# Kernel optimization log

Measured on AMD Instinct MI355X. Metric: run time of the kernel, lower is better.

Reference implementation:

```python
import jax, jax.numpy as jnp
import numpy as np

H1 = 768
H2 = 768
B, LQ, LK = 8, 1024, 1024


def setup_inputs() -> dict:
    key = jax.random.key(0)
    ks = jax.random.split(key, 12)
    s1 = 1.0 / np.sqrt(H1)
    s2 = 1.0 / np.sqrt(H2)
    # weights stored as [in, out] (equivalent to torch Linear weight.T)
    return {
        "tensor1": jax.random.normal(ks[0], (B, LQ, H1), jnp.float32),
        "tensor2": jax.random.normal(ks[1], (B, LK, H2), jnp.float32),
        "Wq": jax.random.uniform(ks[2], (3, H1, H2), jnp.float32, -s1, s1),
        "bq": jax.random.uniform(ks[3], (3, H2), jnp.float32, -s1, s1),
        "Wk": jax.random.uniform(ks[4], (3, H2, H2), jnp.float32, -s2, s2),
        "bk": jax.random.uniform(ks[5], (3, H2), jnp.float32, -s2, s2),
        "Wv": jax.random.uniform(ks[6], (3, H2, H2), jnp.float32, -s2, s2),
        "bv": jax.random.uniform(ks[7], (3, H2), jnp.float32, -s2, s2),
        "Wp": jax.random.uniform(ks[8], (3 * H2, H2), jnp.float32, -1.0 / np.sqrt(3 * H2), 1.0 / np.sqrt(3 * H2)),
        "bp": jax.random.uniform(ks[9], (H2,), jnp.float32, -1.0 / np.sqrt(3 * H2), 1.0 / np.sqrt(3 * H2)),
    }


def reference(tensor1, tensor2, Wq, bq, Wk, bk, Wv, bv, Wp, bp):
    # Three independent cross-attention heads, stacked on leading axis h=3.
    q = jnp.einsum("bqd,hde->hbqe", tensor1, Wq) + bq[:, None, None, :]  # [3,B,LQ,H2]
    k = jnp.einsum("bkd,hde->hbke", tensor2, Wk) + bk[:, None, None, :]  # [3,B,LK,H2]
    v = jnp.einsum("bkd,hde->hbke", tensor2, Wv) + bv[:, None, None, :]  # [3,B,LK,H2]
    scores = jnp.einsum("hbqe,hbke->hbqk", q, k)  # NOTE: no 1/sqrt(d) scaling, per original
    weights = jax.nn.softmax(scores, axis=-1)
    ctx = jnp.einsum("hbqk,hbke->hbqe", weights, v)  # [3,B,LQ,H2]
    # concat heads along feature dim -> [B,LQ,3*H2]
    multi = jnp.transpose(ctx, (1, 2, 0, 3)).reshape(ctx.shape[1], ctx.shape[2], -1)
    # project_multihead: ReLU then Linear
    return jax.nn.relu(multi) @ Wp + bp
```

## Files before the change

kernel.cpp:

```cpp
#include <hip/hip_runtime.h>
#include <hip/hip_bf16.h>


typedef _Float16 f16;
typedef __attribute__((ext_vector_type(8))) _Float16 f16x8;
typedef __attribute__((ext_vector_type(4))) float f32x4;
typedef __attribute__((ext_vector_type(4))) short s16x4;

#define DI __device__ __forceinline__

DI short f2hs(float f){
  f16 h = (f16)f;
  return __builtin_bit_cast(short, h);
}
DI float hs2f(short s){
  return (float)__builtin_bit_cast(f16, s);
}

DI f32x4 mfma16(f16x8 a, f16x8 b, f32x4 c){
  return __builtin_amdgcn_mfma_f32_16x16x32_f16(a, b, c, 0, 0, 0);
}

#define GLL16(gp, lp) __builtin_amdgcn_global_load_lds( \
    (const __attribute__((address_space(1))) unsigned int*)(gp), \
    (__attribute__((address_space(3))) unsigned int*)(lp), 16, 0, 0)

__global__ void pre_fused_kernel(
    const float* __restrict__ t1, const float* __restrict__ t2,
    short* __restrict__ t1b, short* __restrict__ t2b,
    const float* __restrict__ Wq, const float* __restrict__ Wk,
    short* __restrict__ WqH, short* __restrict__ WkH,
    const float* __restrict__ Wv, const float* __restrict__ Wp,
    short* __restrict__ WvT, short* __restrict__ WpT,
    const float* __restrict__ bq, float* __restrict__ wvb)
{
  __shared__ float tile[32][33];
  int bid = blockIdx.x;
  const int tid = threadIdx.x;

  if (bid < 12288){
    int i = bid*256 + tid;
    const float* in = (i < 1572864) ? t1 : t2;
    short* out = (i < 1572864) ? t1b : t2b;
    int j = (i < 1572864) ? i : i - 1572864;
    f32x4 v = ((const f32x4*)in)[j];
    s16x4 o;
    o[0]=f2hs(v[0]); o[1]=f2hs(v[1]); o[2]=f2hs(v[2]); o[3]=f2hs(v[3]);
    ((s16x4*)out)[j] = o;
    return;
  }
  bid -= 12288;
  if (bid < 3456){
    int i = bid*256 + tid;
    const float* in = (i < 442368) ? Wq : Wk;
    short* out = (i < 442368) ? WqH : WkH;
    int j = (i < 442368) ? i : i - 442368;
    f32x4 v = ((const f32x4*)in)[j];
    s16x4 o;
    o[0]=f2hs(v[0]); o[1]=f2hs(v[1]); o[2]=f2hs(v[2]); o[3]=f2hs(v[3]);
    ((s16x4*)out)[j] = o;
    return;
  }
  bid -= 3456;
  if (bid < 3456){
    const int bz = bid / 1728, rem = bid % 1728;
    const int by = rem / 24, bx = rem % 24;
    const float* in; short* out; int R, r0;
    if (bz == 0){
      int hd = by / 24;
      in = Wv + (long)hd*768*768; out = WvT + (long)hd*768*768;
      R = 768; r0 = (by % 24) * 32;
    } else {
      in = Wp; out = WpT; R = 2304; r0 = by * 32;
    }
    int c0 = bx * 32;
    int tx = tid & 31, ty = tid >> 5;
    #pragma unroll
    for (int k=0;k<4;k++)
      tile[ty + k*8][tx] = in[(long)(r0 + ty + k*8) * 768 + c0 + tx];
    __syncthreads();
    #pragma unroll
    for (int k=0;k<4;k++)
      out[(long)(c0 + ty + k*8) * R + r0 + tx] = f2hs(tile[tx][ty + k*8]);
    return;
  }
  bid -= 3456;
  {
    const int h = bid / 8, chunk = bid % 8;
    const int wave = tid>>6, lane = tid&63;
    const float* bql = bq + h*768 + lane*12;
    float bv[12];
    #pragma unroll
    for (int e=0;e<12;e++) bv[e] = bql[e];
    for (int r = 0; r < 24; r++){
      int d = chunk*96 + r*4 + wave;
      const float* row = Wk + ((long)h*768 + d)*768 + lane*12;
      float s = 0.f;
      #pragma unroll
      for (int e=0;e<12;e++) s += row[e] * bv[e];
      s += __shfl_xor(s, 1);
      s += __shfl_xor(s, 2);
      s += __shfl_xor(s, 4);
      s += __shfl_xor(s, 8);
      s += __shfl_xor(s, 16);
      s += __shfl_xor(s, 32);
      if (lane == 0) wvb[h*768 + d] = s;
    }
  }
}

DI void gemm_tile64(const short* __restrict__ A, const short* __restrict__ Bt, int K,
                    int m0, int n0, short* As, short* Bs, f32x4 (&acc)[4][4])
{
  const int tid = threadIdx.x, wave = tid>>6, lane = tid&63;
  const int wm = wave>>1, wn = wave&1;
  const int fl = lane&15, fq = lane>>4;
  const int srow = lane>>2;
  const int scol = ((lane&3) ^ ((lane>>3)&3))*8;
  const int rs   = (fq ^ ((fl>>1)&3))*8;
  for (int kk=0; kk<K; kk+=64){
    __syncthreads();
    #pragma unroll
    for (int c=0;c<2;c++)
      #pragma unroll
      for (int r=0;r<2;r++){
        const int rb = r*64 + wave*16;
        GLL16(A  + (long)(m0+rb+srow)*K + kk + c*32 + scol, As + c*4096 + rb*32);
        GLL16(Bt + (long)(n0+rb+srow)*K + kk + c*32 + scol, Bs + c*4096 + rb*32);
      }
    __syncthreads();
    #pragma unroll
    for (int c=0;c<2;c++){
      f16x8 a[4];
      #pragma unroll
      for (int i=0;i<4;i++) a[i] = *(const f16x8*)(As + c*4096 + (wm*64+i*16+fl)*32 + rs);
      #pragma unroll
      for (int j=0;j<4;j++){
        f16x8 b = *(const f16x8*)(Bs + c*4096 + (wn*64+j*16+fl)*32 + rs);
        #pragma unroll
        for (int i=0;i<4;i++) acc[i][j] = mfma16(a[i], b, acc[i][j]);
      }
    }
  }
}

__global__ __launch_bounds__(256,2) void gemm_m_kernel(
    const short* __restrict__ WqH, const short* __restrict__ WkH, short* __restrict__ Mt)
{
  __shared__ short As[8192];
  __shared__ short Bs[8192];
  const int h = blockIdx.z;
  const int m0 = blockIdx.x*128, n0 = blockIdx.y*128;
  const int tid = threadIdx.x, wave = tid>>6, lane = tid&63;
  const int wm = wave>>1, wn = wave&1;
  const int fl = lane&15, fq = lane>>4;

  f32x4 vz = {0.f,0.f,0.f,0.f};
  f32x4 acc[4][4];
  #pragma unroll
  for (int i=0;i<4;i++)
    #pragma unroll
    for (int j=0;j<4;j++) acc[i][j] = vz;

  gemm_tile64(WqH + (long)h*768*768, WkH + (long)h*768*768, 768, m0, n0, As, Bs, acc);

  short* outp = Mt + (long)h*768*768;
  #pragma unroll
  for (int j=0;j<4;j++){
    int col = n0 + wn*64 + j*16 + fl;
    #pragma unroll
    for (int i=0;i<4;i++){
      int row = m0 + wm*64 + i*16 + fq*4;
      s16x4 pack;
      #pragma unroll
      for (int r=0;r<4;r++) pack[r] = f2hs(acc[i][j][r]);
      *(s16x4*)(outp + (long)col*768 + row) = pack;
    }
  }
}

__global__ __launch_bounds__(256,2) void gemm_gv_kernel(
    const short* __restrict__ t1b, const short* __restrict__ t2b,
    const short* __restrict__ Mt, const short* __restrict__ WvT,
    const float* __restrict__ wv, const float* __restrict__ bv,
    short* __restrict__ Gb, short* __restrict__ Vtb)
{
  __shared__ short As[8192];
  __shared__ short Bs[8192];
  const int z = blockIdx.z;
  const int h = z % 3, which = z / 3;
  const short* A  = (which==0) ? t1b : t2b;
  const short* Bt = ((which==0)?Mt:WvT) + (long)h*768*768;
  const int m0 = blockIdx.x*128, n0 = blockIdx.y*128;
  const int tid = threadIdx.x, wave = tid>>6, lane = tid&63;
  const int wm = wave>>1, wn = wave&1;
  const int fl = lane&15, fq = lane>>4;

  f32x4 vz = {0.f,0.f,0.f,0.f};
  f32x4 acc[4][4];
  #pragma unroll
  for (int i=0;i<4;i++)
    #pragma unroll
    for (int j=0;j<4;j++) acc[i][j] = vz;

  gemm_tile64(A, Bt, 768, m0, n0, As, Bs, acc);

  if (which == 0){
    const float* bias = wv + h*768;
    short* outp = Gb + (long)h*8192*768;
    #pragma unroll
    for (int j=0;j<4;j++){
      int col = n0 + wn*64 + j*16 + fl;
      float bb = bias[col];
      #pragma unroll
      for (int i=0;i<4;i++){
        int row = m0 + wm*64 + i*16 + fq*4;
        #pragma unroll
        for (int r=0;r<4;r++)
          outp[(long)(row+r)*768 + col] = f2hs(acc[i][j][r] + bb);
      }
    }
  } else {
    const float* bias = bv + h*768;
    const int bidx = m0 >> 10;
    const int lk0  = m0 & 1023;
    short* outp = Vtb + (long)(h*8 + bidx)*768*1024;
    #pragma unroll
    for (int j=0;j<4;j++){
      int e = n0 + wn*64 + j*16 + fl;
      float bb = bias[e];
      #pragma unroll
      for (int i=0;i<4;i++){
        int lk = lk0 + wm*64 + i*16 + fq*4;
        s16x4 pack;
        #pragma unroll
        for (int r=0;r<4;r++) pack[r] = f2hs(acc[i][j][r] + bb);
        *(s16x4*)(outp + (long)e*1024 + lk) = pack;
      }
    }
  }
}

__global__ __launch_bounds__(256,2) void qk_exp_kernel(
    const short* __restrict__ Gb, const short* __restrict__ t2b,
    short* __restrict__ P, float* __restrict__ Mx, float* __restrict__ Lx)
{
  __shared__ short As[8192];
  __shared__ short Bs[8192];
  __shared__ float red0[2][2][64];
  __shared__ float red1[2][2][64];
  const int id = blockIdx.x;
  const int xcd = id & 7, s_ = id >> 3;
  const int hb = xcd*3 + (s_ >> 6);
  const int inner = s_ & 63;
  const int qt = inner & 7, ct = inner >> 3;
  const int h = hb >> 3, b = hb & 7;
  const int tid = threadIdx.x, wave = tid>>6, lane = tid&63;
  const int wm = wave>>1, wn = wave&1;
  const int fl = lane&15, fq = lane>>4;
  const short* Abase = Gb + ((long)h*8192 + b*1024)*768;
  const short* Bbase = t2b + (long)b*1024*768;

  f32x4 vz = {0.f,0.f,0.f,0.f};
  f32x4 acc[4][4];
  #pragma unroll
  for (int i=0;i<4;i++)
    #pragma unroll
    for (int j=0;j<4;j++) acc[i][j] = vz;

  gemm_tile64(Abase, Bbase, 768, qt*128, ct*128, As, Bs, acc);

  float mt[4][4];
  #pragma unroll
  for (int i=0;i<4;i++)
    #pragma unroll
    for (int r=0;r<4;r++){
      float m = acc[i][0][r];
      #pragma unroll
      for (int j=1;j<4;j++) m = fmaxf(m, acc[i][j][r]);
      m = fmaxf(m, __shfl_xor(m, 1));
      m = fmaxf(m, __shfl_xor(m, 2));
      m = fmaxf(m, __shfl_xor(m, 4));
      m = fmaxf(m, __shfl_xor(m, 8));
      mt[i][r] = m;
      if (fl == 0) red0[wn][wm][i*16 + fq*4 + r] = m;
    }
  __syncthreads();
  #pragma unroll
  for (int i=0;i<4;i++)
    #pragma unroll
    for (int r=0;r<4;r++)
      mt[i][r] = fmaxf(red0[0][wm][i*16 + fq*4 + r], red0[1][wm][i*16 + fq*4 + r]);

  #pragma unroll
  for (int i=0;i<4;i++)
    #pragma unroll
    for (int r=0;r<4;r++){
      float s = 0.f;
      #pragma unroll
      for (int j=0;j<4;j++){
        float p = __expf(acc[i][j][r] - mt[i][r]);
        acc[i][j][r] = p;
        s += p;
      }
      s += __shfl_xor(s, 1);
      s += __shfl_xor(s, 2);
      s += __shfl_xor(s, 4);
      s += __shfl_xor(s, 8);
      if (fl == 0) red1[wn][wm][i*16 + fq*4 + r] = s;
    }
  __syncthreads();

  #pragma unroll
  for (int j=0;j<4;j++){
    int c = ct*128 + wn*64 + j*16 + fl;
    #pragma unroll
    for (int i=0;i<4;i++){
      int q = qt*128 + wm*64 + i*16 + fq*4;
      #pragma unroll
      for (int r=0;r<4;r++)
        P[((long)hb*1024 + q + r)*1024 + c] = f2hs(acc[i][j][r]);
    }
  }
  if (fl == 0 && wn == 0){
    long aux = ((long)(hb*8 + ct))*1024 + qt*128;
    #pragma unroll
    for (int i=0;i<4;i++)
      #pragma unroll
      for (int r=0;r<4;r++){
        int row = wm*64 + i*16 + fq*4 + r;
        Mx[aux + row] = mt[i][r];
        Lx[aux + row] = red1[0][wm][row & 63] + red1[1][wm][row & 63];
      }
  }
}

__global__ __launch_bounds__(256,2) void pv_kernel(
    const short* __restrict__ P, const short* __restrict__ Vtb,
    const float* __restrict__ Mx, const float* __restrict__ Lx, short* __restrict__ multi)
{
  __shared__ short As[8192];
  __shared__ short Bs[8192];
  __shared__ float scl[8][128];
  const int id = blockIdx.x;
  const int xcd = id & 7, s_ = id >> 3;
  const int hb = xcd*3 + s_/48;
  const int inner = s_ % 48;
  const int qt = inner & 7, et = inner >> 3;
  const int h = hb >> 3, b = hb & 7;
  const int tid = threadIdx.x, wave = tid>>6, lane = tid&63;
  const int wm = wave>>1, wn = wave&1;
  const int fl = lane&15, fq = lane>>4;
  const int srow = lane>>2;
  const int scol = ((lane&3) ^ ((lane>>3)&3))*8;
  const int rs   = (fq ^ ((fl>>1)&3))*8;
  const short* Abase = P + (long)hb*1024*1024 + (long)(qt*128)*1024;
  const short* Bbase = Vtb + (long)hb*768*1024 + (long)(et*128)*1024;

  if (tid < 128){
    long a0 = ((long)(hb*8))*1024 + qt*128 + tid;
    float m[8], l[8];
    #pragma unroll
    for (int t=0;t<8;t++){ m[t] = Mx[a0 + t*1024]; l[t] = Lx[a0 + t*1024]; }
    float mg = m[0];
    #pragma unroll
    for (int t=1;t<8;t++) mg = fmaxf(mg, m[t]);
    float lg = 0.f;
    #pragma unroll
    for (int t=0;t<8;t++) lg += l[t] * __expf(m[t] - mg);
    float inv = 1.0f / lg;
    #pragma unroll
    for (int t=0;t<8;t++) scl[t][tid] = __expf(m[t] - mg) * inv;
  }
  __syncthreads();

  f32x4 vz = {0.f,0.f,0.f,0.f};
  f32x4 acc[4][4];
  #pragma unroll
  for (int i=0;i<4;i++)
    #pragma unroll
    for (int j=0;j<4;j++) acc[i][j] = vz;

  for (int ct=0; ct<8; ct++){
    f16 s[4];
    #pragma unroll
    for (int i=0;i<4;i++) s[i] = (f16)scl[ct][wm*64 + i*16 + fl];
    #pragma unroll
    for (int t=0;t<2;t++){
      const int kk = ct*128 + t*64;
      __syncthreads();
      #pragma unroll
      for (int c=0;c<2;c++)
        #pragma unroll
        for (int r=0;r<2;r++){
          const int rb = r*64 + wave*16;
          GLL16(Abase + (long)(rb+srow)*1024 + kk + c*32 + scol, As + c*4096 + rb*32);
          GLL16(Bbase + (long)(rb+srow)*1024 + kk + c*32 + scol, Bs + c*4096 + rb*32);
        }
      __syncthreads();
      #pragma unroll
      for (int c=0;c<2;c++){
        f16x8 a[4];
        #pragma unroll
        for (int i=0;i<4;i++){
          f16x8 av = *(const f16x8*)(As + c*4096 + (wm*64+i*16+fl)*32 + rs);
          f16x8 sv;
          #pragma unroll
          for (int e=0;e<8;e++) sv[e] = s[i];
          a[i] = av * sv;
        }
        #pragma unroll
        for (int j=0;j<4;j++){
          f16x8 bvv = *(const f16x8*)(Bs + c*4096 + (wn*64+j*16+fl)*32 + rs);
          #pragma unroll
          for (int i=0;i<4;i++) acc[i][j] = mfma16(a[i], bvv, acc[i][j]);
        }
      }
    }
  }

  short* mp = multi + (long)(b*1024 + qt*128)*2304 + h*768 + et*128;
  #pragma unroll
  for (int j=0;j<4;j++){
    int e = wn*64 + j*16 + fl;
    #pragma unroll
    for (int i=0;i<4;i++){
      int q = wm*64 + i*16 + fq*4;
      #pragma unroll
      for (int r=0;r<4;r++)
        mp[(long)(q+r)*2304 + e] = f2hs(fmaxf(acc[i][j][r], 0.f));
    }
  }
}

__global__ __launch_bounds__(256,2) void gemm_out_kernel(
    const short* __restrict__ A, const short* __restrict__ Bt,
    const float* __restrict__ bias, float* __restrict__ out)
{
  __shared__ short As[8192];
  __shared__ short Bs[8192];
  const int m0 = blockIdx.x*128, n0 = blockIdx.y*128;
  const int tid = threadIdx.x, wave = tid>>6, lane = tid&63;
  const int wm = wave>>1, wn = wave&1;
  const int fl = lane&15, fq = lane>>4;

  f32x4 vz = {0.f,0.f,0.f,0.f};
  f32x4 acc[4][4];
  #pragma unroll
  for (int i=0;i<4;i++)
    #pragma unroll
    for (int j=0;j<4;j++) acc[i][j] = vz;

  gemm_tile64(A, Bt, 2304, m0, n0, As, Bs, acc);

  #pragma unroll
  for (int j=0;j<4;j++){
    int col = n0 + wn*64 + j*16 + fl;
    float bb = bias[col];
    #pragma unroll
    for (int i=0;i<4;i++){
      int row = m0 + wm*64 + i*16 + fq*4;
      #pragma unroll
      for (int r=0;r<4;r++)
        out[(long)(row+r)*768 + col] = acc[i][j][r] + bb;
    }
  }
}

extern "C" void kernel_launch(void* const* d_in, const int* in_sizes, int n_in,
                              void* d_out, int out_size, void* d_ws, size_t ws_size,
                              hipStream_t stream)
{
  const float* t1 = (const float*)d_in[0];
  const float* t2 = (const float*)d_in[1];
  const float* Wq = (const float*)d_in[2];
  const float* bq = (const float*)d_in[3];
  const float* Wk = (const float*)d_in[4];
  const float* Wv = (const float*)d_in[6];
  const float* bv = (const float*)d_in[7];
  const float* Wp = (const float*)d_in[8];
  const float* bp = (const float*)d_in[9];
  float* out = (float*)d_out;

  char* ws = (char*)d_ws;
  size_t off = 0;
  auto carve = [&](size_t bytes){ void* p = ws + off; off += (bytes + 255) & ~(size_t)255; return p; };
  short* t1b = (short*)carve(8L*1024*768*2);
  short* t2b = (short*)carve(8L*1024*768*2);
  short* WqH = (short*)carve(3L*768*768*2);
  short* WkH = (short*)carve(3L*768*768*2);
  short* WvT = (short*)carve(3L*768*768*2);
  short* WpT = (short*)carve(768L*2304*2);
  short* Mt  = (short*)carve(3L*768*768*2);
  short* Gb  = (short*)carve(3L*8192*768*2);
  short* Vtb = (short*)carve(3L*8*768*1024*2);
  short* Pb  = (short*)carve(24L*1024*1024*2);
  float* Mx  = (float*)carve(24L*8*1024*4);
  float* Lx  = (float*)carve(24L*8*1024*4);
  float* wvb = (float*)carve(3L*768*4);
  short* multib = Gb;

  pre_fused_kernel<<<19224, 256, 0, stream>>>(t1, t2, t1b, t2b, Wq, Wk, WqH, WkH,
                                              Wv, Wp, WvT, WpT, bq, wvb);
  gemm_m_kernel<<<dim3(6,6,3), 256, 0, stream>>>(WqH, WkH, Mt);
  gemm_gv_kernel<<<dim3(64,6,6), 256, 0, stream>>>(t1b, t2b, Mt, WvT, wvb, bv, Gb, Vtb);
  qk_exp_kernel<<<1536, 256, 0, stream>>>(Gb, t2b, Pb, Mx, Lx);
  pv_kernel<<<1152, 256, 0, stream>>>(Pb, Vtb, Mx, Lx, multib);
  gemm_out_kernel<<<dim3(64,6,1), 256, 0, stream>>>(multib, WpT, bp, out);
}
```

Before: 382.7 us.

## Fuse Wq·Wk^T GEMM into preprocessing kernel, converting weights on the fly

Removes the separate gemm_m kernel and the fp32→fp16 conversion pass for Wq/Wk. The M = Wq·Wk^T product is computed directly inside the fused preprocessing kernel, loading fp32 weights and converting them to half while storing to LDS. The GEMM blocks are placed first in the grid so they overlap with the element-wise conversion blocks. This saves one launch and the WqH/WkH round trip. In exchange, the preprocessing kernel gains large LDS usage, which may lower occupancy for the many small conversion blocks.

```diff
diff --git a/kernel.cpp b/kernel.cpp
--- a/kernel.cpp
+++ b/kernel.cpp
@@ -6,15 +6,13 @@
 typedef __attribute__((ext_vector_type(8))) _Float16 f16x8;
 typedef __attribute__((ext_vector_type(4))) float f32x4;
 typedef __attribute__((ext_vector_type(4))) short s16x4;
+typedef __attribute__((ext_vector_type(8))) short s16x8;
 
 #define DI __device__ __forceinline__
 
 DI short f2hs(float f){
   f16 h = (f16)f;
   return __builtin_bit_cast(short, h);
-}
-DI float hs2f(short s){
-  return (float)__builtin_bit_cast(f16, s);
 }
 
 DI f32x4 mfma16(f16x8 a, f16x8 b, f32x4 c){
@@ -29,39 +27,110 @@
     const float* __restrict__ t1, const float* __restrict__ t2,
     short* __restrict__ t1b, short* __restrict__ t2b,
     const float* __restrict__ Wq, const float* __restrict__ Wk,
-    short* __restrict__ WqH, short* __restrict__ WkH,
+    short* __restrict__ Mt,
     const float* __restrict__ Wv, const float* __restrict__ Wp,
     short* __restrict__ WvT, short* __restrict__ WpT,
     const float* __restrict__ bq, float* __restrict__ wvb)
 {
+  __shared__ short As[8192];
+  __shared__ short Bs[8192];
   __shared__ float tile[32][33];
   int bid = blockIdx.x;
   const int tid = threadIdx.x;
 
-  if (bid < 12288){
-    int i = bid*256 + tid;
-    const float* in = (i < 1572864) ? t1 : t2;
-    short* out = (i < 1572864) ? t1b : t2b;
-    int j = (i < 1572864) ? i : i - 1572864;
-    f32x4 v = ((const f32x4*)in)[j];
-    s16x4 o;
-    o[0]=f2hs(v[0]); o[1]=f2hs(v[1]); o[2]=f2hs(v[2]); o[3]=f2hs(v[3]);
-    ((s16x4*)out)[j] = o;
+  if (bid < 108){
+    const int h = bid / 36, rem = bid % 36;
+    const int m0 = (rem / 6) * 128, n0 = (rem % 6) * 128;
+    const float* A  = Wq + (long)h*768*768;
+    const float* Bt = Wk + (long)h*768*768;
+    const int wave = tid>>6, lane = tid&63;
+    const int wm = wave>>1, wn = wave&1;
+    const int fl = lane&15, fq = lane>>4;
+    const int srow = lane>>2, sl = lane&3;
+    const int gco = (sl ^ ((srow>>1)&3))*8;
+    const int rs  = (fq ^ ((fl>>1)&3))*8;
+
+    f32x4 vz = {0.f,0.f,0.f,0.f};
+    f32x4 acc[4][4];
+    #pragma unroll
+    for (int i=0;i<4;i++)
+      #pragma unroll
+      for (int j=0;j<4;j++) acc[i][j] = vz;
+
+    for (int kk=0; kk<768; kk+=64){
+      __syncthreads();
+      #pragma unroll
+      for (int c=0;c<2;c++)
+        #pragma unroll
+        for (int r=0;r<2;r++){
+          const int row = r*64 + wave*16 + srow;
+          const int gc  = kk + c*32 + gco;
+          const float* pa = A  + (long)(m0+row)*768 + gc;
+          const float* pb = Bt + (long)(n0+row)*768 + gc;
+          f32x4 a0 = *(const f32x4*)pa, a1 = *(const f32x4*)(pa+4);
+          f32x4 b0 = *(const f32x4*)pb, b1 = *(const f32x4*)(pb+4);
+          s16x8 ha, hb;
+          #pragma unroll
+          for (int e=0;e<4;e++){ ha[e]=f2hs(a0[e]); ha[4+e]=f2hs(a1[e]);
+                                 hb[e]=f2hs(b0[e]); hb[4+e]=f2hs(b1[e]); }
+          *(s16x8*)(As + c*4096 + row*32 + sl*8) = ha;
+          *(s16x8*)(Bs + c*4096 + row*32 + sl*8) = hb;
+        }
+      __syncthreads();
+      #pragma unroll
+      for (int c=0;c<2;c++){
+        f16x8 a[4];
+        #pragma unroll
+        for (int i=0;i<4;i++) a[i] = *(const f16x8*)(As + c*4096 + (wm*64+i*16+fl)*32 + rs);
+        #pragma unroll
+        for (int j=0;j<4;j++){
+          f16x8 b = *(const f16x8*)(Bs + c*4096 + (wn*64+j*16+fl)*32 + rs);
+          #pragma unroll
+          for (int i=0;i<4;i++) acc[i][j] = mfma16(a[i], b, acc[i][j]);
+        }
+      }
+    }
+
+    short* outp = Mt + (long)h*768*768;
+    #pragma unroll
+    for (int j=0;j<4;j++){
+      int col = n0 + wn*64 + j*16 + fl;
+      #pragma unroll
+      for (int i=0;i<4;i++){
+        int row = m0 + wm*64 + i*16 + fq*4;
+        s16x4 pack;
+        #pragma unroll
+        for (int r=0;r<4;r++) pack[r] = f2hs(acc[i][j][r]);
+        *(s16x4*)(outp + (long)col*768 + row) = pack;
+      }
+    }
     return;
   }
-  bid -= 12288;
-  if (bid < 3456){
-    int i = bid*256 + tid;
-    const float* in = (i < 442368) ? Wq : Wk;
-    short* out = (i < 442368) ? WqH : WkH;
-    int j = (i < 442368) ? i : i - 442368;
-    f32x4 v = ((const f32x4*)in)[j];
-    s16x4 o;
-    o[0]=f2hs(v[0]); o[1]=f2hs(v[1]); o[2]=f2hs(v[2]); o[3]=f2hs(v[3]);
-    ((s16x4*)out)[j] = o;
+  bid -= 108;
+  if (bid < 24){
+    const int h = bid / 8, chunk = bid % 8;
+    const int wave = tid>>6, lane = tid&63;
+    const float* bql = bq + h*768 + lane*12;
+    float bv[12];
+    #pragma unroll
+    for (int e=0;e<12;e++) bv[e] = bql[e];
+    for (int r = 0; r < 24; r++){
+      int d = chunk*96 + r*4 + wave;
+      const float* row = Wk + ((long)h*768 + d)*768 + lane*12;
+      float s = 0.f;
+      #pragma unroll
+      for (int e=0;e<12;e++) s += row[e] * bv[e];
+      s += __shfl_xor(s, 1);
+      s += __shfl_xor(s, 2);
+      s += __shfl_xor(s, 4);
+      s += __shfl_xor(s, 8);
+      s += __shfl_xor(s, 16);
+      s += __shfl_xor(s, 32);
+      if (lane == 0) wvb[h*768 + d] = s;
+    }
     return;
   }
-  bid -= 3456;
+  bid -= 24;
   if (bid < 3456){
     const int bz = bid / 1728, rem = bid % 1728;
     const int by = rem / 24, bx = rem % 24;
@@ -86,26 +155,14 @@
   }
   bid -= 3456;
   {
-    const int h = bid / 8, chunk = bid % 8;
-    const int wave = tid>>6, lane = tid&63;
-    const float* bql = bq + h*768 + lane*12;
-    float bv[12];
-    #pragma unroll
-    for (int e=0;e<12;e++) bv[e] = bql[e];
-    for (int r = 0; r < 24; r++){
-      int d = chunk*96 + r*4 + wave;
-      const float* row = Wk + ((long)h*768 + d)*768 + lane*12;
-      float s = 0.f;
-      #pragma unroll
-      for (int e=0;e<12;e++) s += row[e] * bv[e];
-      s += __shfl_xor(s, 1);
-      s += __shfl_xor(s, 2);
-      s += __shfl_xor(s, 4);
-      s += __shfl_xor(s, 8);
-      s += __shfl_xor(s, 16);
-      s += __shfl_xor(s, 32);
-      if (lane == 0) wvb[h*768 + d] = s;
-    }
+    int i = bid*256 + tid;
+    const float* in = (i < 1572864) ? t1 : t2;
+    short* out = (i < 1572864) ? t1b : t2b;
+    int j = (i < 1572864) ? i : i - 1572864;
+    f32x4 v = ((const f32x4*)in)[j];
+    s16x4 o;
+    o[0]=f2hs(v[0]); o[1]=f2hs(v[1]); o[2]=f2hs(v[2]); o[3]=f2hs(v[3]);
+    ((s16x4*)out)[j] = o;
   }
 }
 
@@ -140,41 +197,6 @@
         #pragma unroll
         for (int i=0;i<4;i++) acc[i][j] = mfma16(a[i], b, acc[i][j]);
       }
-    }
-  }
-}
-
-__global__ __launch_bounds__(256,2) void gemm_m_kernel(
-    const short* __restrict__ WqH, const short* __restrict__ WkH, short* __restrict__ Mt)
-{
-  __shared__ short As[8192];
-  __shared__ short Bs[8192];
-  const int h = blockIdx.z;
-  const int m0 = blockIdx.x*128, n0 = blockIdx.y*128;
-  const int tid = threadIdx.x, wave = tid>>6, lane = tid&63;
-  const int wm = wave>>1, wn = wave&1;
-  const int fl = lane&15, fq = lane>>4;
-
-  f32x4 vz = {0.f,0.f,0.f,0.f};
-  f32x4 acc[4][4];
-  #pragma unroll
-  for (int i=0;i<4;i++)
-    #pragma unroll
-    for (int j=0;j<4;j++) acc[i][j] = vz;
-
-  gemm_tile64(WqH + (long)h*768*768, WkH + (long)h*768*768, 768, m0, n0, As, Bs, acc);
-
-  short* outp = Mt + (long)h*768*768;
-  #pragma unroll
-  for (int j=0;j<4;j++){
-    int col = n0 + wn*64 + j*16 + fl;
-    #pragma unroll
-    for (int i=0;i<4;i++){
-      int row = m0 + wm*64 + i*16 + fq*4;
-      s16x4 pack;
-      #pragma unroll
-      for (int r=0;r<4;r++) pack[r] = f2hs(acc[i][j][r]);
-      *(s16x4*)(outp + (long)col*768 + row) = pack;
     }
   }
 }
@@ -487,8 +509,6 @@
   auto carve = [&](size_t bytes){ void* p = ws + off; off += (bytes + 255) & ~(size_t)255; return p; };
   short* t1b = (short*)carve(8L*1024*768*2);
   short* t2b = (short*)carve(8L*1024*768*2);
-  short* WqH = (short*)carve(3L*768*768*2);
-  short* WkH = (short*)carve(3L*768*768*2);
   short* WvT = (short*)carve(3L*768*768*2);
   short* WpT = (short*)carve(768L*2304*2);
   short* Mt  = (short*)carve(3L*768*768*2);
@@ -500,9 +520,8 @@
   float* wvb = (float*)carve(3L*768*4);
   short* multib = Gb;
 
-  pre_fused_kernel<<<19224, 256, 0, stream>>>(t1, t2, t1b, t2b, Wq, Wk, WqH, WkH,
+  pre_fused_kernel<<<15876, 256, 0, stream>>>(t1, t2, t1b, t2b, Wq, Wk, Mt,
                                               Wv, Wp, WvT, WpT, bq, wvb);
-  gemm_m_kernel<<<dim3(6,6,3), 256, 0, stream>>>(WqH, WkH, Mt);
   gemm_gv_kernel<<<dim3(64,6,6), 256, 0, stream>>>(t1b, t2b, Mt, WvT, wvb, bv, Gb, Vtb);
   qk_exp_kernel<<<1536, 256, 0, stream>>>(Gb, t2b, Pb, Mx, Lx);
   pv_kernel<<<1152, 256, 0, stream>>>(Pb, Vtb, Mx, Lx, multib);
```

Result: faster. 364.4 us, median of 2 (-4.8%).
